# Kernel tuning notes

Measured on AMD Instinct MI355X. Metric: run time of the kernel, lower is better.

Reference implementation:

```python
import jax, jax.numpy as jnp
import numpy as np

B, L, C = 4, 2048, 2048
NH, HD, K = 32, 64, 16  # num_heads, head_dim, inner chunk size
LR = 1.0
EPS = 1e-6


def ln_fwd(x, w, b):
    # F.layer_norm over last dim (biased variance), eps=1e-6
    mu = x.mean(-1, keepdims=True)
    var = x.var(-1, keepdims=True)
    xhat = (x - mu) * jax.lax.rsqrt(var + EPS)
    return w * xhat + b


def ln_fused_l2_bwd(x, target, w, b):
    # grad wrt x of 0.5*||LN(x;w,b) - target||^2 fused with LN fwd
    D = x.shape[-1]
    mu = x.mean(-1, keepdims=True)
    var = x.var(-1, keepdims=True)
    std = jnp.sqrt(var + EPS)
    xhat = (x - mu) / std
    y = w * xhat + b
    g = (y - target) * w  # dL/d(xhat)
    return (D * g - g.sum(-1, keepdims=True) - xhat * (g * xhat).sum(-1, keepdims=True)) / (D * std)


def _inner_scan(XC, XB, XA, coeff, W1, b1, lnw, lnb):
    # per (batch, head): XC/XB/XA [n_chunk,K,HD], coeff [n_chunk,K,1], W1 [HD,HD], b1 [1,HD], lnw/lnb [HD]
    mask = jnp.tril(jnp.ones((K, K), XC.dtype))

    def step(carry, inp):
        W1c, b1c = carry
        xc, xb, xa, co = inp
        Z1 = xb @ W1c + b1c                       # [K,HD]
        grad = ln_fused_l2_bwd(Z1, xa - xb, lnw, lnb)
        Attn1 = mask * (xc @ xb.T)                # [K,K] causal
        b1_bar = b1c - (co * mask) @ grad         # [K,HD]
        Z1_bar = xc @ W1c - (co * Attn1) @ grad + b1_bar
        W1n = W1c - (co[-1] * xb).T @ grad        # fast-weight update with last coeff
        b1n = b1_bar[-1:]
        out = xc + ln_fwd(Z1_bar, lnw, lnb)       # post-LN residual
        return (W1n, b1n), out

    _, ys = jax.lax.scan(step, (W1, b1), (XC, XB, XA, coeff))
    return ys.reshape(-1, HD)  # [L,HD]


def setup_inputs() -> dict:
    key = jax.random.key(0)
    ks = jax.random.split(key, 9)
    s = 0.02
    return {
        'hidden_states': jax.random.normal(ks[0], (B, L, C), jnp.float32),
        'Wq': jax.random.normal(ks[1], (C, NH * HD), jnp.float32) * s,
        'Wk': jax.random.normal(ks[2], (C, NH * HD), jnp.float32) * s,
        'Wv': jax.random.normal(ks[3], (C, NH * HD), jnp.float32) * s,
        'Wo': jax.random.normal(ks[4], (NH * HD, C), jnp.float32) * s,
        'ilr_w': jax.random.normal(ks[5], (C, NH), jnp.float32) * s,
        'ilr_b': jnp.zeros((NH,), jnp.float32),
        'ln_weight': jnp.ones((NH, HD), jnp.float32),
        'ln_bias': jnp.zeros((NH, HD), jnp.float32),
        'W1': jax.random.normal(ks[6], (NH, HD, HD), jnp.float32) * s,
        'b1': jnp.zeros((NH, 1, HD), jnp.float32),
    }


def reference(hidden_states, Wq, Wk, Wv, Wo, ilr_w, ilr_b, ln_weight, ln_bias, W1, b1):
    n_chunk = L // K

    def split(x):  # [B,L,NH*HD] -> [B,NH,n_chunk,K,HD]
        return x.reshape(B, n_chunk, K, NH, HD).transpose(0, 3, 1, 2, 4)

    XC = split(hidden_states @ Wq)
    XB = split(hidden_states @ Wk)
    XA = split(hidden_states @ Wv)

    # sigmoid-gated per-token learning rates
    ilr = jax.nn.sigmoid(hidden_states @ ilr_w + ilr_b)          # [B,L,NH]
    ilr = ilr.reshape(B, n_chunk, K, NH).transpose(0, 3, 1, 2)[..., None]  # [B,NH,n_chunk,K,1]
    token_idx = 1.0 / jnp.arange(1, K + 1, dtype=jnp.float32)
    coeff = (LR * token_idx).reshape(1, 1, 1, K, 1) * ilr / HD

    per_head = jax.vmap(_inner_scan, in_axes=(0, 0, 0, 0, 0, 0, 0, 0))
    per_batch = jax.vmap(per_head, in_axes=(0, 0, 0, 0, None, None, None, None))
    XCW = per_batch(XC, XB, XA, coeff, W1, b1, ln_weight, ln_bias)  # [B,NH,L,HD]
    XCW = XCW.transpose(0, 2, 1, 3).reshape(B, L, NH * HD)
    return XCW @ Wo
```

## Files before the change

kernel.cpp:

```cpp
#include <hip/hip_runtime.h>
#include <hip/hip_bf16.h>

typedef __attribute__((ext_vector_type(8))) short bf16x8;
typedef __attribute__((ext_vector_type(4))) float f32x4;
typedef __attribute__((ext_vector_type(8))) unsigned short u16x8;
typedef __attribute__((ext_vector_type(4))) unsigned short u16x4;
typedef unsigned short u16;

#define AS1(p) ((__attribute__((address_space(1))) void*)(p))
#define AS3(p) ((__attribute__((address_space(3))) void*)(p))
#define GLL16(g, l) __builtin_amdgcn_global_load_lds(AS1(g), AS3(l), 16, 0, 0)

__device__ __forceinline__ u16 f2bf(float x) {
  return __builtin_bit_cast(u16, __float2bfloat16(x));
}
__device__ __forceinline__ float bf2f(u16 u) {
  return __builtin_bit_cast(float, ((unsigned)u) << 16);
}
__device__ __forceinline__ unsigned pk2(float a, float b) {
  return (unsigned)f2bf(a) | ((unsigned)f2bf(b) << 16);
}
__device__ __forceinline__ f32x4 mfma16(bf16x8 a, bf16x8 b, f32x4 c) {
  return __builtin_amdgcn_mfma_f32_16x16x32_bf16(a, b, c, 0, 0, 0);
}
#define DPPADD(x, ctrl)                                                            \
  ((x) + __builtin_bit_cast(float, __builtin_amdgcn_update_dpp(                    \
             0, __builtin_bit_cast(int, (x)), (ctrl), 0xf, 0xf, true)))
__device__ __forceinline__ float rsum16(float x) {
  x = DPPADD(x, 0x128);
  x = DPPADD(x, 0x124);
  x = DPPADD(x, 0x122);
  x = DPPADD(x, 0x121);
  return x;
}
__device__ __forceinline__ void dsfence() { __builtin_amdgcn_sched_barrier(0x7F); }
template <typename T>
__device__ __forceinline__ void lds_st(u16* p, T v) {
  __builtin_memcpy((void*)p, &v, sizeof(T));
}
template <typename T>
__device__ __forceinline__ T lds_ld(const u16* p) {
  T v;
  __builtin_memcpy(&v, (const void*)p, sizeof(T));
  return v;
}

__global__ __launch_bounds__(256) void conv_bf16(const float* __restrict__ in,
                                                 u16* __restrict__ out) {
  size_t g = (size_t)blockIdx.x * 256 + threadIdx.x;
  const float4* p = reinterpret_cast<const float4*>(in) + g * 2;
  float4 a = p[0], b = p[1];
  u16x8 r;
  r[0] = f2bf(a.x); r[1] = f2bf(a.y); r[2] = f2bf(a.z); r[3] = f2bf(a.w);
  r[4] = f2bf(b.x); r[5] = f2bf(b.y); r[6] = f2bf(b.z); r[7] = f2bf(b.w);
  *reinterpret_cast<u16x8*>(out + g * 8) = r;
}

__global__ __launch_bounds__(256) void wt_conv(const float* __restrict__ W,
                                               u16* __restrict__ Wt, int Kd, int N) {
  __shared__ float t[64][65];
  const int n0 = blockIdx.x * 64, k0 = blockIdx.y * 64;
  const int tx = threadIdx.x & 63, ty = threadIdx.x >> 6;
#pragma unroll
  for (int rr = 0; rr < 16; ++rr) {
    int r = rr * 4 + ty;
    t[r][tx] = W[(size_t)(k0 + r) * N + n0 + tx];
  }
  __syncthreads();
#pragma unroll
  for (int rr = 0; rr < 16; ++rr) {
    int r = rr * 4 + ty;
    Wt[(size_t)(n0 + r) * Kd + k0 + tx] = f2bf(t[tx][r]);
  }
}

__global__ __launch_bounds__(256) void ilr_strip(const float* __restrict__ ilr_w,
                                                 u16* __restrict__ WcatT) {
  int g = blockIdx.x * 256 + threadIdx.x;
  int p = g >> 11, k = g & 2047;
  float v = (p < 32) ? ilr_w[k * 32 + p] : 0.f;
  WcatT[(size_t)(6144 + p) * 2048 + k] = f2bf(v);
}

__device__ __forceinline__ void stage_pair(const u16* __restrict__ A, const u16* __restrict__ Bt,
                                           u16* As, u16* Bs, int Kd, int mT, int nT, int kt,
                                           int tid) {
#pragma unroll
  for (int r = 0; r < 2; ++r) {
    int e = r * 2048 + tid * 8;
    int row = e >> 5, kk = e & 31;
    GLL16(A + (size_t)(mT + row) * Kd + kt + kk, As + e);
    GLL16(Bt + (size_t)(nT + row) * Kd + kt + kk, Bs + e);
  }
}

template <int MODE>
__global__ __launch_bounds__(256) void gemm_bt(const u16* __restrict__ A,
                                               const u16* __restrict__ Bt, int M, int N, int Kd,
                                               u16* __restrict__ O0, u16* __restrict__ O1,
                                               u16* __restrict__ O2,
                                               float* __restrict__ coeffOut,
                                               const float* __restrict__ ilrb,
                                               float* __restrict__ Cout) {
  __shared__ __align__(16) u16 As[2][4096];
  __shared__ __align__(16) u16 Bs[2][4096];
  const int tid = threadIdx.x;
  const int lane = tid & 63;
  const int wid = tid >> 6;
  const int wr = wid >> 1, wc = wid & 1;
  const int l15 = lane & 15, l4 = lane >> 4;
  const int mT = blockIdx.y << 7, nT = blockIdx.x << 7;

  f32x4 acc[4][4];
#pragma unroll
  for (int m = 0; m < 4; ++m)
#pragma unroll
    for (int n = 0; n < 4; ++n) acc[m][n] = (f32x4){0.f, 0.f, 0.f, 0.f};

  stage_pair(A, Bt, &As[0][0], &Bs[0][0], Kd, mT, nT, 0, tid);
  const int nIter = Kd >> 5;
  const int aoff = (wr * 64 + l15) * 32 + l4 * 8;
  const int boff = (wc * 64 + l15) * 32 + l4 * 8;
#pragma unroll 1
  for (int it = 0; it < nIter; ++it) {
    const int cur = it & 1;
    __syncthreads();
    if (it + 1 < nIter)
      stage_pair(A, Bt, &As[cur ^ 1][0], &Bs[cur ^ 1][0], Kd, mT, nT, (it + 1) << 5, tid);
    bf16x8 av[4], bv[4];
#pragma unroll
    for (int x = 0; x < 4; ++x) {
      av[x] = *reinterpret_cast<const bf16x8*>(&As[cur][aoff + x * 512]);
      bv[x] = *reinterpret_cast<const bf16x8*>(&Bs[cur][boff + x * 512]);
    }
#pragma unroll
    for (int m = 0; m < 4; ++m)
#pragma unroll
      for (int n = 0; n < 4; ++n) acc[m][n] = mfma16(av[m], bv[n], acc[m][n]);
  }
#pragma unroll
  for (int m = 0; m < 4; ++m) {
#pragma unroll
    for (int n = 0; n < 4; ++n) {
      const int col = nT + wc * 64 + n * 16 + l15;
#pragma unroll
      for (int e = 0; e < 4; ++e) {
        const int row = mT + wr * 64 + m * 16 + l4 * 4 + e;
        float v = acc[m][n][e];
        if constexpr (MODE == 1) {
          Cout[(size_t)row * N + col] = v;
        } else {
          const int bb = row >> 11, lt = row & 2047;
          if (col < 6144) {
            const int mat = col >> 11;
            u16* base = (mat == 0) ? O0 : ((mat == 1) ? O1 : O2);
            const int hh = (col >> 6) & 31, dd = col & 63;
            base[(((size_t)(bb * 32 + hh)) * 2048 + lt) * 64 + dd] = f2bf(v);
          } else {
            const int h3 = col - 6144;
            if (h3 < 32) {
              const float x = v + ilrb[h3];
              const float sig = 1.f / (1.f + expf(-x));
              const int tok = lt & 15;
              coeffOut[((size_t)(bb * 32 + h3)) * 2048 + lt] =
                  sig * (1.f / (64.f * (float)(tok + 1)));
            }
          }
        }
      }
    }
  }
  (void)M;
}

__global__ __launch_bounds__(64) void ttt_scan(
    const u16* __restrict__ XC, const u16* __restrict__ XB, const u16* __restrict__ XA,
    const float* __restrict__ coeff, const float* __restrict__ lnw_g,
    const float* __restrict__ lnb_g, const float* __restrict__ W1g,
    const float* __restrict__ b1g, u16* __restrict__ XCW) {
  const int bh = blockIdx.x;
  const int b = bh >> 5, h = bh & 31;
  const int lane = threadIdx.x & 63;
  const int l15 = lane & 15, l4 = lane >> 4;
  const bool klo = (l4 < 2);

  const u16* xbb = XB + (size_t)bh * 131072;
  const u16* xcb = XC + (size_t)bh * 131072;
  const u16* xab = XA + (size_t)bh * 131072;
  const float* cob = coeff + (size_t)bh * 2048;

  float lnw4[4], lnb4[4], b1m[4];
#pragma unroll
  for (int cb = 0; cb < 4; ++cb) {
    lnw4[cb] = lnw_g[h * 64 + cb * 16 + l15];
    lnb4[cb] = lnb_g[h * 64 + cb * 16 + l15];
    b1m[cb] = b1g[h * 64 + cb * 16 + l15];
  }
  f32x4 mW[4][4];
#pragma unroll
  for (int kb = 0; kb < 4; ++kb)
#pragma unroll
    for (int cb = 0; cb < 4; ++cb)
#pragma unroll
      for (int e = 0; e < 4; ++e)
        mW[kb][cb][e] = W1g[(size_t)h * 4096 + (kb * 16 + l4 * 4 + e) * 64 + cb * 16 + l15];

  __shared__ __align__(16) u16 w1L[64 * 72];
  __shared__ __align__(16) u16 xbTs[64 * 24];
  __shared__ __align__(16) u16 gTs[64 * 24];
  __shared__ __align__(16) u16 ptw[256];

  uint4 nfb0, nfb1, nfc0, nfc1;
  float nco[4], nco15;
  u16 nxa[4][4], nxbC[4][4], nxcC[4][4], nxv[16];
  const int fo = l15 * 128 + l4 * 16;
#define PREFETCH(cc)                                                                 \
  do {                                                                               \
    const char* pb = (const char*)(xbb + (cc) * 1024);                               \
    const char* pc = (const char*)(xcb + (cc) * 1024);                               \
    nfb0 = *(const uint4*)(pb + fo); nfb1 = *(const uint4*)(pb + fo + 64);           \
    nfc0 = *(const uint4*)(pc + fo); nfc1 = *(const uint4*)(pc + fo + 64);           \
    const u16* xap_ = xab + (cc) * 1024;                                             \
    const u16* xbp_ = xbb + (cc) * 1024;                                             \
    const u16* xcp_ = xcb + (cc) * 1024;                                             \
    _Pragma("unroll") for (int cb = 0; cb < 4; ++cb)                                 \
        _Pragma("unroll") for (int e = 0; e < 4; ++e) {                              \
      const int idx = (l4 * 4 + e) * 64 + cb * 16 + l15;                             \
      nxa[cb][e] = xap_[idx];                                                        \
      nxbC[cb][e] = xbp_[idx];                                                       \
      nxcC[cb][e] = xcp_[idx];                                                       \
    }                                                                                \
    _Pragma("unroll") for (int r = 0; r < 16; ++r) nxv[r] = xbp_[r * 64 + lane];     \
    _Pragma("unroll") for (int e = 0; e < 4; ++e) nco[e] = cob[(cc) * 16 + l4 * 4 + e]; \
    nco15 = cob[(cc) * 16 + 15];                                                     \
  } while (0)

  PREFETCH(0);

#pragma unroll 1
  for (int c = 0; c < 128; ++c) {
    const bf16x8 xbr0 = __builtin_bit_cast(bf16x8, nfb0);
    const bf16x8 xbr1 = __builtin_bit_cast(bf16x8, nfb1);
    const bf16x8 xcr0 = __builtin_bit_cast(bf16x8, nfc0);
    const bf16x8 xcr1 = __builtin_bit_cast(bf16x8, nfc1);
    float co_own[4];
#pragma unroll
    for (int e = 0; e < 4; ++e) co_own[e] = nco[e];
    const float co15 = nco15;
    float tgt[4][4], xcC[4][4];
#pragma unroll
    for (int cb = 0; cb < 4; ++cb)
#pragma unroll
      for (int e = 0; e < 4; ++e) {
        tgt[cb][e] = bf2f(nxa[cb][e]) - bf2f(nxbC[cb][e]);
        xcC[cb][e] = bf2f(nxcC[cb][e]);
      }
    u16 xv[16];
#pragma unroll
    for (int r = 0; r < 16; ++r) xv[r] = nxv[r];

    {
      const int cc = (c < 127) ? (c + 1) : 127;
      PREFETCH(cc);
    }

    f32x4 p = {0.f, 0.f, 0.f, 0.f};
    p = mfma16(xcr0, xbr0, p);
    p = mfma16(xcr1, xbr1, p);
#pragma unroll
    for (int e = 0; e < 4; ++e) {
      const int i = l4 * 4 + e;
      const float v = (l15 <= i) ? p[e] * (-co_own[e]) : 0.f;
      lds_st<u16>(&ptw[i * 16 + l15], f2bf(v));
    }

    {
      const float s = -co15;
#pragma unroll
      for (int r2 = 0; r2 < 4; ++r2) {
        u16x4 w;
#pragma unroll
        for (int i = 0; i < 4; ++i) w[i] = f2bf(bf2f(xv[r2 * 4 + i]) * s);
        lds_st<u16x4>(&xbTs[lane * 24 + r2 * 4], w);
      }
    }

#pragma unroll
    for (int kb = 0; kb < 4; ++kb)
#pragma unroll
      for (int cb = 0; cb < 4; ++cb) {
        u16x4 w;
#pragma unroll
        for (int e = 0; e < 4; ++e) w[e] = f2bf(mW[kb][cb][e]);
        lds_st<u16x4>(&w1L[(cb * 16 + l15) * 72 + kb * 16 + l4 * 4], w);
      }
    dsfence();
    bf16x8 w1f[4][2];
#pragma unroll
    for (int cb = 0; cb < 4; ++cb)
#pragma unroll
      for (int s = 0; s < 2; ++s)
        w1f[cb][s] = lds_ld<bf16x8>(&w1L[(cb * 16 + l15) * 72 + s * 32 + l4 * 8]);
    dsfence();

    f32x4 z[4];
#pragma unroll
    for (int cb = 0; cb < 4; ++cb) {
      f32x4 acc = {b1m[cb], b1m[cb], b1m[cb], b1m[cb]};
      acc = mfma16(xbr0, w1f[cb][0], acc);
      z[cb] = mfma16(xbr1, w1f[cb][1], acc);
    }
    f32x4 o2[4];
#pragma unroll
    for (int cb = 0; cb < 4; ++cb) {
      f32x4 acc = {0.f, 0.f, 0.f, 0.f};
      acc = mfma16(xcr0, w1f[cb][0], acc);
      o2[cb] = mfma16(xcr1, w1f[cb][1], acc);
    }

    float xhat[4][4], gr[4][4];
#pragma unroll
    for (int e = 0; e < 4; ++e) {
      float s1 = z[0][e] + z[1][e] + z[2][e] + z[3][e];
      float s2 = z[0][e] * z[0][e] + z[1][e] * z[1][e] + z[2][e] * z[2][e] + z[3][e] * z[3][e];
      s1 = rsum16(s1);
      s2 = rsum16(s2);
      const float mu = s1 * 0.015625f;
      const float var = fmaxf(s2 * 0.015625f - mu * mu, 0.f);
      const float rstd = rsqrtf(var + 1e-6f);
      float gloc[4];
#pragma unroll
      for (int cb = 0; cb < 4; ++cb) {
        xhat[cb][e] = (z[cb][e] - mu) * rstd;
        gloc[cb] = (fmaf(lnw4[cb], xhat[cb][e], lnb4[cb]) - tgt[cb][e]) * lnw4[cb];
      }
      float gs = gloc[0] + gloc[1] + gloc[2] + gloc[3];
      float gx = gloc[0] * xhat[0][e] + gloc[1] * xhat[1][e] + gloc[2] * xhat[2][e] +
                 gloc[3] * xhat[3][e];
      gs = rsum16(gs);
      gx = rsum16(gx);
#pragma unroll
      for (int cb = 0; cb < 4; ++cb)
        gr[cb][e] = (64.f * gloc[cb] - gs - xhat[cb][e] * gx) * (rstd * 0.015625f);
    }

    float gtot[4], lower[4];
#pragma unroll
    for (int cb = 0; cb < 4; ++cb) {
      const float T = gr[cb][0] + gr[cb][1] + gr[cb][2] + gr[cb][3];
      const float t1 = __shfl_xor(T, 16, 64);
      const float t2 = __shfl_xor(T, 32, 64);
      const float t3 = __shfl_xor(t1, 32, 64);
      gtot[cb] = T + t1 + t2 + t3;
      lower[cb] = ((l4 & 1) ? t1 : 0.f) + ((l4 & 2) ? (t2 + t3) : 0.f);
    }

#pragma unroll
    for (int cb = 0; cb < 4; ++cb) {
      uint2 w = {pk2(gr[cb][0], gr[cb][1]), pk2(gr[cb][2], gr[cb][3])};
      lds_st<uint2>(&gTs[(cb * 16 + l15) * 24 + l4 * 4], w);
    }
    dsfence();
    bf16x8 gf[4];
    const bf16x8 zero8 = {};
#pragma unroll
    for (int cb = 0; cb < 4; ++cb) {
      bf16x8 v = lds_ld<bf16x8>(&gTs[(cb * 16 + l15) * 24 + (l4 & 1) * 8]);
      gf[cb] = klo ? v : zero8;
    }
    bf16x8 ptf;
    {
      bf16x8 v = lds_ld<bf16x8>(&ptw[l15 * 16 + (l4 & 1) * 8]);
      ptf = klo ? v : zero8;
    }
    dsfence();

#pragma unroll
    for (int cb = 0; cb < 4; ++cb) o2[cb] = mfma16(ptf, gf[cb], o2[cb]);
    float ov[4][4];
#pragma unroll
    for (int cb = 0; cb < 4; ++cb) {
      float pfx = lower[cb];
#pragma unroll
      for (int e = 0; e < 4; ++e) {
        pfx += gr[cb][e];
        ov[cb][e] = o2[cb][e] + fmaf(-co_own[e], pfx, b1m[cb]);
      }
    }
#pragma unroll
    for (int e = 0; e < 4; ++e) {
      float s1 = ov[0][e] + ov[1][e] + ov[2][e] + ov[3][e];
      float s2 = ov[0][e] * ov[0][e] + ov[1][e] * ov[1][e] + ov[2][e] * ov[2][e] +
                 ov[3][e] * ov[3][e];
      s1 = rsum16(s1);
      s2 = rsum16(s2);
      const float mu = s1 * 0.015625f;
      const float var = fmaxf(s2 * 0.015625f - mu * mu, 0.f);
      const float rstd = rsqrtf(var + 1e-6f);
      const size_t rowg = (size_t)(b * 2048 + c * 16 + l4 * 4 + e) * 2048 + h * 64;
#pragma unroll
      for (int cb = 0; cb < 4; ++cb) {
        const float y = xcC[cb][e] + fmaf(lnw4[cb], (ov[cb][e] - mu) * rstd, lnb4[cb]);
        XCW[rowg + cb * 16 + l15] = f2bf(y);
      }
    }

    bf16x8 xbtf[4];
#pragma unroll
    for (int kb = 0; kb < 4; ++kb) {
      bf16x8 v = lds_ld<bf16x8>(&xbTs[(kb * 16 + l15) * 24 + (l4 & 1) * 8]);
      xbtf[kb] = klo ? v : zero8;
    }
    dsfence();
#pragma unroll
    for (int kb = 0; kb < 4; ++kb)
#pragma unroll
      for (int cb = 0; cb < 4; ++cb) mW[kb][cb] = mfma16(xbtf[kb], gf[cb], mW[kb][cb]);
#pragma unroll
    for (int cb = 0; cb < 4; ++cb) b1m[cb] = fmaf(-co15, gtot[cb], b1m[cb]);
    dsfence();
  }
#undef PREFETCH
}

extern "C" void kernel_launch(void* const* d_in, const int* in_sizes, int n_in, void* d_out,
                              int out_size, void* d_ws, size_t ws_size, hipStream_t stream) {
  const float* hs = (const float*)d_in[0];
  const float* Wq = (const float*)d_in[1];
  const float* Wk = (const float*)d_in[2];
  const float* Wv = (const float*)d_in[3];
  const float* Wo = (const float*)d_in[4];
  const float* ilr_w = (const float*)d_in[5];
  const float* ilr_b = (const float*)d_in[6];
  const float* lnw = (const float*)d_in[7];
  const float* lnb = (const float*)d_in[8];
  const float* W1 = (const float*)d_in[9];
  const float* b1 = (const float*)d_in[10];
  float* out = (float*)d_out;

  if (ws_size < 93847552u) return;
  char* ws = (char*)d_ws;
  u16* hsb = (u16*)(ws + 0);
  u16* WcatT = (u16*)(ws + 33554432);
  u16* XCbf = (u16*)(ws + 59244544);
  float* coeffb = (float*)(ws + 92798976);
  u16* XCW = hsb;
  u16* WoT = (u16*)(ws + 33554432);
  u16* XBbf = (u16*)d_out;
  u16* XAbf = (u16*)((char*)d_out + 33554432);

  conv_bf16<<<8192, 256, 0, stream>>>(hs, hsb);
  wt_conv<<<dim3(32, 32), 256, 0, stream>>>(Wq, WcatT, 2048, 2048);
  wt_conv<<<dim3(32, 32), 256, 0, stream>>>(Wk, WcatT + (size_t)2048 * 2048, 2048, 2048);
  wt_conv<<<dim3(32, 32), 256, 0, stream>>>(Wv, WcatT + (size_t)4096 * 2048, 2048, 2048);
  ilr_strip<<<1024, 256, 0, stream>>>(ilr_w, WcatT);

  gemm_bt<0><<<dim3(49, 64), 256, 0, stream>>>(hsb, WcatT, 8192, 6272, 2048, XCbf, XBbf, XAbf,
                                               coeffb, ilr_b, nullptr);
  wt_conv<<<dim3(32, 32), 256, 0, stream>>>(Wo, WoT, 2048, 2048);
  ttt_scan<<<128, 64, 0, stream>>>(XCbf, XBbf, XAbf, coeffb, lnw, lnb, W1, b1, XCW);
  gemm_bt<1><<<dim3(16, 64), 256, 0, stream>>>(XCW, WoT, 8192, 2048, 2048, nullptr, nullptr,
                                               nullptr, nullptr, nullptr, out);

  (void)in_sizes; (void)n_in; (void)out_size;
}
```

Before: 750.3 us.

## Interleave two independent head sequences per wavefront in TTT scan kernel

The scan kernel now processes two (batch, head) sequences per 64-thread block, with their independent dependency chains interleaved inside one chunk loop, and the grid shrinks from 128 to 64 blocks. The aim is to hide MFMA, LDS and shuffle latency of the serial per-chunk recurrence through instruction-level parallelism across the two streams. The scalar element loads for XA, XB and XC are no longer prefetched one chunk ahead; they are issued in the current iteration. In exchange, only 64 CUs are used instead of 128, register pressure roughly doubles, and the moved loads may expose memory latency.

```diff
diff --git a/kernel.cpp b/kernel.cpp
--- a/kernel.cpp
+++ b/kernel.cpp
@@ -173,254 +173,290 @@
   (void)M;
 }
 
-__global__ __launch_bounds__(64) void ttt_scan(
+__global__ __launch_bounds__(64, 1) void ttt_scan(
     const u16* __restrict__ XC, const u16* __restrict__ XB, const u16* __restrict__ XA,
     const float* __restrict__ coeff, const float* __restrict__ lnw_g,
     const float* __restrict__ lnb_g, const float* __restrict__ W1g,
     const float* __restrict__ b1g, u16* __restrict__ XCW) {
-  const int bh = blockIdx.x;
-  const int b = bh >> 5, h = bh & 31;
+  const int q = blockIdx.x;
+  const int h = q & 31;
   const int lane = threadIdx.x & 63;
   const int l15 = lane & 15, l4 = lane >> 4;
   const bool klo = (l4 < 2);
 
-  const u16* xbb = XB + (size_t)bh * 131072;
-  const u16* xcb = XC + (size_t)bh * 131072;
-  const u16* xab = XA + (size_t)bh * 131072;
-  const float* cob = coeff + (size_t)bh * 2048;
-
-  float lnw4[4], lnb4[4], b1m[4];
+  const u16 *xbb[2], *xcb[2], *xab[2];
+  const float* cob[2];
+  int bseq[2];
+#pragma unroll
+  for (int s = 0; s < 2; ++s) {
+    const int bh = q + s * 64;
+    bseq[s] = bh >> 5;
+    xbb[s] = XB + (size_t)bh * 131072;
+    xcb[s] = XC + (size_t)bh * 131072;
+    xab[s] = XA + (size_t)bh * 131072;
+    cob[s] = coeff + (size_t)bh * 2048;
+  }
+
+  float lnw4[4], lnb4[4];
 #pragma unroll
   for (int cb = 0; cb < 4; ++cb) {
     lnw4[cb] = lnw_g[h * 64 + cb * 16 + l15];
     lnb4[cb] = lnb_g[h * 64 + cb * 16 + l15];
-    b1m[cb] = b1g[h * 64 + cb * 16 + l15];
-  }
-  f32x4 mW[4][4];
-#pragma unroll
-  for (int kb = 0; kb < 4; ++kb)
-#pragma unroll
-    for (int cb = 0; cb < 4; ++cb)
-#pragma unroll
-      for (int e = 0; e < 4; ++e)
-        mW[kb][cb][e] = W1g[(size_t)h * 4096 + (kb * 16 + l4 * 4 + e) * 64 + cb * 16 + l15];
-
-  __shared__ __align__(16) u16 w1L[64 * 72];
-  __shared__ __align__(16) u16 xbTs[64 * 24];
-  __shared__ __align__(16) u16 gTs[64 * 24];
-  __shared__ __align__(16) u16 ptw[256];
-
-  uint4 nfb0, nfb1, nfc0, nfc1;
-  float nco[4], nco15;
-  u16 nxa[4][4], nxbC[4][4], nxcC[4][4], nxv[16];
+  }
+  float b1m[2][4];
+  f32x4 mW[2][4][4];
+#pragma unroll
+  for (int s = 0; s < 2; ++s) {
+#pragma unroll
+    for (int cb = 0; cb < 4; ++cb) b1m[s][cb] = b1g[h * 64 + cb * 16 + l15];
+#pragma unroll
+    for (int kb = 0; kb < 4; ++kb)
+#pragma unroll
+      for (int cb = 0; cb < 4; ++cb)
+#pragma unroll
+        for (int e = 0; e < 4; ++e)
+          mW[s][kb][cb][e] =
+              W1g[(size_t)h * 4096 + (kb * 16 + l4 * 4 + e) * 64 + cb * 16 + l15];
+  }
+
+  __shared__ __align__(16) u16 w1L[2][64 * 72];
+  __shared__ __align__(16) u16 xbTs[2][64 * 24];
+  __shared__ __align__(16) u16 gTs[2][64 * 24];
+  __shared__ __align__(16) u16 ptw[2][256];
+
+  uint4 nfb0[2], nfb1[2], nfc0[2], nfc1[2];
+  float nco[2][4], nco15[2];
   const int fo = l15 * 128 + l4 * 16;
-#define PREFETCH(cc)                                                                 \
-  do {                                                                               \
-    const char* pb = (const char*)(xbb + (cc) * 1024);                               \
-    const char* pc = (const char*)(xcb + (cc) * 1024);                               \
-    nfb0 = *(const uint4*)(pb + fo); nfb1 = *(const uint4*)(pb + fo + 64);           \
-    nfc0 = *(const uint4*)(pc + fo); nfc1 = *(const uint4*)(pc + fo + 64);           \
-    const u16* xap_ = xab + (cc) * 1024;                                             \
-    const u16* xbp_ = xbb + (cc) * 1024;                                             \
-    const u16* xcp_ = xcb + (cc) * 1024;                                             \
-    _Pragma("unroll") for (int cb = 0; cb < 4; ++cb)                                 \
-        _Pragma("unroll") for (int e = 0; e < 4; ++e) {                              \
-      const int idx = (l4 * 4 + e) * 64 + cb * 16 + l15;                             \
-      nxa[cb][e] = xap_[idx];                                                        \
-      nxbC[cb][e] = xbp_[idx];                                                       \
-      nxcC[cb][e] = xcp_[idx];                                                       \
-    }                                                                                \
-    _Pragma("unroll") for (int r = 0; r < 16; ++r) nxv[r] = xbp_[r * 64 + lane];     \
-    _Pragma("unroll") for (int e = 0; e < 4; ++e) nco[e] = cob[(cc) * 16 + l4 * 4 + e]; \
-    nco15 = cob[(cc) * 16 + 15];                                                     \
+#define PFRAG(s, cc)                                                                  \
+  do {                                                                                \
+    const char* pb = (const char*)(xbb[s] + (cc) * 1024);                             \
+    const char* pc = (const char*)(xcb[s] + (cc) * 1024);                             \
+    nfb0[s] = *(const uint4*)(pb + fo); nfb1[s] = *(const uint4*)(pb + fo + 64);      \
+    nfc0[s] = *(const uint4*)(pc + fo); nfc1[s] = *(const uint4*)(pc + fo + 64);      \
+    _Pragma("unroll") for (int e = 0; e < 4; ++e)                                     \
+        nco[s][e] = cob[s][(cc) * 16 + l4 * 4 + e];                                   \
+    nco15[s] = cob[s][(cc) * 16 + 15];                                                \
   } while (0)
 
-  PREFETCH(0);
+#pragma unroll
+  for (int s = 0; s < 2; ++s) PFRAG(s, 0);
 
 #pragma unroll 1
   for (int c = 0; c < 128; ++c) {
-    const bf16x8 xbr0 = __builtin_bit_cast(bf16x8, nfb0);
-    const bf16x8 xbr1 = __builtin_bit_cast(bf16x8, nfb1);
-    const bf16x8 xcr0 = __builtin_bit_cast(bf16x8, nfc0);
-    const bf16x8 xcr1 = __builtin_bit_cast(bf16x8, nfc1);
-    float co_own[4];
-#pragma unroll
-    for (int e = 0; e < 4; ++e) co_own[e] = nco[e];
-    const float co15 = nco15;
-    float tgt[4][4], xcC[4][4];
-#pragma unroll
-    for (int cb = 0; cb < 4; ++cb)
-#pragma unroll
-      for (int e = 0; e < 4; ++e) {
-        tgt[cb][e] = bf2f(nxa[cb][e]) - bf2f(nxbC[cb][e]);
-        xcC[cb][e] = bf2f(nxcC[cb][e]);
-      }
-    u16 xv[16];
-#pragma unroll
-    for (int r = 0; r < 16; ++r) xv[r] = nxv[r];
+    bf16x8 xbr0[2], xbr1[2], xcr0[2], xcr1[2];
+    float co_own[2][4], co15[2];
+#pragma unroll
+    for (int s = 0; s < 2; ++s) {
+      xbr0[s] = __builtin_bit_cast(bf16x8, nfb0[s]);
+      xbr1[s] = __builtin_bit_cast(bf16x8, nfb1[s]);
+      xcr0[s] = __builtin_bit_cast(bf16x8, nfc0[s]);
+      xcr1[s] = __builtin_bit_cast(bf16x8, nfc1[s]);
+#pragma unroll
+      for (int e = 0; e < 4; ++e) co_own[s][e] = nco[s][e];
+      co15[s] = nco15[s];
+    }
+
+    u16 sxa[2][4][4], sxb[2][4][4], sxc[2][4][4], sxv[2][16];
+#pragma unroll
+    for (int s = 0; s < 2; ++s) {
+      const u16* xap_ = xab[s] + c * 1024;
+      const u16* xbp_ = xbb[s] + c * 1024;
+      const u16* xcp_ = xcb[s] + c * 1024;
+#pragma unroll
+      for (int cb = 0; cb < 4; ++cb)
+#pragma unroll
+        for (int e = 0; e < 4; ++e) {
+          const int idx = (l4 * 4 + e) * 64 + cb * 16 + l15;
+          sxa[s][cb][e] = xap_[idx];
+          sxb[s][cb][e] = xbp_[idx];
+          sxc[s][cb][e] = xcp_[idx];
+        }
+#pragma unroll
+      for (int r = 0; r < 16; ++r) sxv[s][r] = xbp_[r * 64 + lane];
+    }
 
     {
       const int cc = (c < 127) ? (c + 1) : 127;
-      PREFETCH(cc);
-    }
-
-    f32x4 p = {0.f, 0.f, 0.f, 0.f};
-    p = mfma16(xcr0, xbr0, p);
-    p = mfma16(xcr1, xbr1, p);
-#pragma unroll
-    for (int e = 0; e < 4; ++e) {
-      const int i = l4 * 4 + e;
-      const float v = (l15 <= i) ? p[e] * (-co_own[e]) : 0.f;
-      lds_st<u16>(&ptw[i * 16 + l15], f2bf(v));
-    }
-
-    {
-      const float s = -co15;
+#pragma unroll
+      for (int s = 0; s < 2; ++s) PFRAG(s, cc);
+    }
+
+#pragma unroll
+    for (int s = 0; s < 2; ++s) {
+      f32x4 p = {0.f, 0.f, 0.f, 0.f};
+      p = mfma16(xcr0[s], xbr0[s], p);
+      p = mfma16(xcr1[s], xbr1[s], p);
+#pragma unroll
+      for (int e = 0; e < 4; ++e) {
+        const int i = l4 * 4 + e;
+        const float v = (l15 <= i) ? p[e] * (-co_own[s][e]) : 0.f;
+        lds_st<u16>(&ptw[s][i * 16 + l15], f2bf(v));
+      }
+    }
+
+#pragma unroll
+    for (int s = 0; s < 2; ++s)
+#pragma unroll
+      for (int kb = 0; kb < 4; ++kb)
+#pragma unroll
+        for (int cb = 0; cb < 4; ++cb) {
+          u16x4 w;
+#pragma unroll
+          for (int e = 0; e < 4; ++e) w[e] = f2bf(mW[s][kb][cb][e]);
+          lds_st<u16x4>(&w1L[s][(cb * 16 + l15) * 72 + kb * 16 + l4 * 4], w);
+        }
+    dsfence();
+    f32x4 z[2][4], o2[2][4];
+#pragma unroll
+    for (int s = 0; s < 2; ++s) {
+      bf16x8 w1f[4][2];
+#pragma unroll
+      for (int cb = 0; cb < 4; ++cb)
+#pragma unroll
+        for (int t = 0; t < 2; ++t)
+          w1f[cb][t] = lds_ld<bf16x8>(&w1L[s][(cb * 16 + l15) * 72 + t * 32 + l4 * 8]);
+#pragma unroll
+      for (int cb = 0; cb < 4; ++cb) {
+        f32x4 a = {b1m[s][cb], b1m[s][cb], b1m[s][cb], b1m[s][cb]};
+        a = mfma16(xbr0[s], w1f[cb][0], a);
+        z[s][cb] = mfma16(xbr1[s], w1f[cb][1], a);
+        f32x4 a2 = {0.f, 0.f, 0.f, 0.f};
+        a2 = mfma16(xcr0[s], w1f[cb][0], a2);
+        o2[s][cb] = mfma16(xcr1[s], w1f[cb][1], a2);
+      }
+    }
+    dsfence();
+
+    float gr[2][4][4];
+#pragma unroll
+    for (int s = 0; s < 2; ++s) {
+#pragma unroll
+      for (int e = 0; e < 4; ++e) {
+        float zz[4];
+#pragma unroll
+        for (int cb = 0; cb < 4; ++cb) zz[cb] = z[s][cb][e];
+        float s1 = zz[0] + zz[1] + zz[2] + zz[3];
+        float s2 = zz[0] * zz[0] + zz[1] * zz[1] + zz[2] * zz[2] + zz[3] * zz[3];
+        s1 = rsum16(s1);
+        s2 = rsum16(s2);
+        const float mu = s1 * 0.015625f;
+        const float var = fmaxf(s2 * 0.015625f - mu * mu, 0.f);
+        const float rstd = rsqrtf(var + 1e-6f);
+        float xh[4], gl[4];
+#pragma unroll
+        for (int cb = 0; cb < 4; ++cb) {
+          xh[cb] = (zz[cb] - mu) * rstd;
+          const float tgt = bf2f(sxa[s][cb][e]) - bf2f(sxb[s][cb][e]);
+          gl[cb] = (fmaf(lnw4[cb], xh[cb], lnb4[cb]) - tgt) * lnw4[cb];
+        }
+        float gs = gl[0] + gl[1] + gl[2] + gl[3];
+        float gx = gl[0] * xh[0] + gl[1] * xh[1] + gl[2] * xh[2] + gl[3] * xh[3];
+        gs = rsum16(gs);
+        gx = rsum16(gx);
+#pragma unroll
+        for (int cb = 0; cb < 4; ++cb)
+          gr[s][cb][e] = (64.f * gl[cb] - gs - xh[cb] * gx) * (rstd * 0.015625f);
+      }
+    }
+
+    float gtot[2][4], lower[2][4];
+#pragma unroll
+    for (int s = 0; s < 2; ++s)
+#pragma unroll
+      for (int cb = 0; cb < 4; ++cb) {
+        const float T = gr[s][cb][0] + gr[s][cb][1] + gr[s][cb][2] + gr[s][cb][3];
+        const float t1 = __shfl_xor(T, 16, 64);
+        const float t2 = __shfl_xor(T, 32, 64);
+        const float t3 = __shfl_xor(t1, 32, 64);
+        gtot[s][cb] = T + t1 + t2 + t3;
+        lower[s][cb] = ((l4 & 1) ? t1 : 0.f) + ((l4 & 2) ? (t2 + t3) : 0.f);
+      }
+
+#pragma unroll
+    for (int s = 0; s < 2; ++s) {
+      const float sc = -co15[s];
 #pragma unroll
       for (int r2 = 0; r2 < 4; ++r2) {
         u16x4 w;
 #pragma unroll
-        for (int i = 0; i < 4; ++i) w[i] = f2bf(bf2f(xv[r2 * 4 + i]) * s);
-        lds_st<u16x4>(&xbTs[lane * 24 + r2 * 4], w);
-      }
-    }
-
-#pragma unroll
-    for (int kb = 0; kb < 4; ++kb)
+        for (int i = 0; i < 4; ++i) w[i] = f2bf(bf2f(sxv[s][r2 * 4 + i]) * sc);
+        lds_st<u16x4>(&xbTs[s][lane * 24 + r2 * 4], w);
+      }
 #pragma unroll
       for (int cb = 0; cb < 4; ++cb) {
-        u16x4 w;
-#pragma unroll
-        for (int e = 0; e < 4; ++e) w[e] = f2bf(mW[kb][cb][e]);
-        lds_st<u16x4>(&w1L[(cb * 16 + l15) * 72 + kb * 16 + l4 * 4], w);
-      }
+        uint2 w = {pk2(gr[s][cb][0], gr[s][cb][1]), pk2(gr[s][cb][2], gr[s][cb][3])};
+        lds_st<uint2>(&gTs[s][(cb * 16 + l15) * 24 + l4 * 4], w);
+      }
+    }
     dsfence();
-    bf16x8 w1f[4][2];
-#pragma unroll
-    for (int cb = 0; cb < 4; ++cb)
-#pragma unroll
-      for (int s = 0; s < 2; ++s)
-        w1f[cb][s] = lds_ld<bf16x8>(&w1L[(cb * 16 + l15) * 72 + s * 32 + l4 * 8]);
+    bf16x8 gf[2][4], ptf[2], xbtf[2][4];
+    const bf16x8 zero8 = {};
+#pragma unroll
+    for (int s = 0; s < 2; ++s) {
+#pragma unroll
+      for (int cb = 0; cb < 4; ++cb) {
+        bf16x8 v = lds_ld<bf16x8>(&gTs[s][(cb * 16 + l15) * 24 + (l4 & 1) * 8]);
+        gf[s][cb] = klo ? v : zero8;
+      }
+      {
+        bf16x8 v = lds_ld<bf16x8>(&ptw[s][l15 * 16 + (l4 & 1) * 8]);
+        ptf[s] = klo ? v : zero8;
+      }
+#pragma unroll
+      for (int kb = 0; kb < 4; ++kb) {
+        bf16x8 v = lds_ld<bf16x8>(&xbTs[s][(kb * 16 + l15) * 24 + (l4 & 1) * 8]);
+        xbtf[s][kb] = klo ? v : zero8;
+      }
+    }
     dsfence();
 
-    f32x4 z[4];
-#pragma unroll
-    for (int cb = 0; cb < 4; ++cb) {
-      f32x4 acc = {b1m[cb], b1m[cb], b1m[cb], b1m[cb]};
-      acc = mfma16(xbr0, w1f[cb][0], acc);
-      z[cb] = mfma16(xbr1, w1f[cb][1], acc);
-    }
-    f32x4 o2[4];
-#pragma unroll
-    for (int cb = 0; cb < 4; ++cb) {
-      f32x4 acc = {0.f, 0.f, 0.f, 0.f};
-      acc = mfma16(xcr0, w1f[cb][0], acc);
-      o2[cb] = mfma16(xcr1, w1f[cb][1], acc);
-    }
-
-    float xhat[4][4], gr[4][4];
-#pragma unroll
-    for (int e = 0; e < 4; ++e) {
-      float s1 = z[0][e] + z[1][e] + z[2][e] + z[3][e];
-      float s2 = z[0][e] * z[0][e] + z[1][e] * z[1][e] + z[2][e] * z[2][e] + z[3][e] * z[3][e];
-      s1 = rsum16(s1);
-      s2 = rsum16(s2);
-      const float mu = s1 * 0.015625f;
-      const float var = fmaxf(s2 * 0.015625f - mu * mu, 0.f);
-      const float rstd = rsqrtf(var + 1e-6f);
-      float gloc[4];
+#pragma unroll
+    for (int s = 0; s < 2; ++s) {
+#pragma unroll
+      for (int cb = 0; cb < 4; ++cb) o2[s][cb] = mfma16(ptf[s], gf[s][cb], o2[s][cb]);
+      float ov[4][4];
 #pragma unroll
       for (int cb = 0; cb < 4; ++cb) {
-        xhat[cb][e] = (z[cb][e] - mu) * rstd;
-        gloc[cb] = (fmaf(lnw4[cb], xhat[cb][e], lnb4[cb]) - tgt[cb][e]) * lnw4[cb];
-      }
-      float gs = gloc[0] + gloc[1] + gloc[2] + gloc[3];
-      float gx = gloc[0] * xhat[0][e] + gloc[1] * xhat[1][e] + gloc[2] * xhat[2][e] +
-                 gloc[3] * xhat[3][e];
-      gs = rsum16(gs);
-      gx = rsum16(gx);
-#pragma unroll
-      for (int cb = 0; cb < 4; ++cb)
-        gr[cb][e] = (64.f * gloc[cb] - gs - xhat[cb][e] * gx) * (rstd * 0.015625f);
-    }
-
-    float gtot[4], lower[4];
-#pragma unroll
-    for (int cb = 0; cb < 4; ++cb) {
-      const float T = gr[cb][0] + gr[cb][1] + gr[cb][2] + gr[cb][3];
-      const float t1 = __shfl_xor(T, 16, 64);
-      const float t2 = __shfl_xor(T, 32, 64);
-      const float t3 = __shfl_xor(t1, 32, 64);
-      gtot[cb] = T + t1 + t2 + t3;
-      lower[cb] = ((l4 & 1) ? t1 : 0.f) + ((l4 & 2) ? (t2 + t3) : 0.f);
-    }
-
-#pragma unroll
-    for (int cb = 0; cb < 4; ++cb) {
-      uint2 w = {pk2(gr[cb][0], gr[cb][1]), pk2(gr[cb][2], gr[cb][3])};
-      lds_st<uint2>(&gTs[(cb * 16 + l15) * 24 + l4 * 4], w);
+        float pfx = lower[s][cb];
+#pragma unroll
+        for (int e = 0; e < 4; ++e) {
+          pfx += gr[s][cb][e];
+          ov[cb][e] = o2[s][cb][e] + fmaf(-co_own[s][e], pfx, b1m[s][cb]);
+        }
+      }
+#pragma unroll
+      for (int e = 0; e < 4; ++e) {
+        float s1 = ov[0][e] + ov[1][e] + ov[2][e] + ov[3][e];
+        float s2 = ov[0][e] * ov[0][e] + ov[1][e] * ov[1][e] + ov[2][e] * ov[2][e] +
+                   ov[3][e] * ov[3][e];
+        s1 = rsum16(s1);
+        s2 = rsum16(s2);
+        const float mu = s1 * 0.015625f;
+        const float var = fmaxf(s2 * 0.015625f - mu * mu, 0.f);
+        const float rstd = rsqrtf(var + 1e-6f);
+        const size_t rowg = (size_t)(bseq[s] * 2048 + c * 16 + l4 * 4 + e) * 2048 + h * 64;
+#pragma unroll
+        for (int cb = 0; cb < 4; ++cb) {
+          const float y =
+              bf2f(sxc[s][cb][e]) + fmaf(lnw4[cb], (ov[cb][e] - mu) * rstd, lnb4[cb]);
+          XCW[rowg + cb * 16 + l15] = f2bf(y);
+        }
+      }
+    }
+
+#pragma unroll
+    for (int s = 0; s < 2; ++s) {
+#pragma unroll
+      for (int kb = 0; kb < 4; ++kb)
+#pragma unroll
+        for (int cb = 0; cb < 4; ++cb)
+          mW[s][kb][cb] = mfma16(xbtf[s][kb], gf[s][cb], mW[s][kb][cb]);
+#pragma unroll
+      for (int cb = 0; cb < 4; ++cb) b1m[s][cb] = fmaf(-co15[s], gtot[s][cb], b1m[s][cb]);
     }
     dsfence();
-    bf16x8 gf[4];
-    const bf16x8 zero8 = {};
-#pragma unroll
-    for (int cb = 0; cb < 4; ++cb) {
-      bf16x8 v = lds_ld<bf16x8>(&gTs[(cb * 16 + l15) * 24 + (l4 & 1) * 8]);
-      gf[cb] = klo ? v : zero8;
-    }
-    bf16x8 ptf;
-    {
-      bf16x8 v = lds_ld<bf16x8>(&ptw[l15 * 16 + (l4 & 1) * 8]);
-      ptf = klo ? v : zero8;
-    }
-    dsfence();
-
-#pragma unroll
-    for (int cb = 0; cb < 4; ++cb) o2[cb] = mfma16(ptf, gf[cb], o2[cb]);
-    float ov[4][4];
-#pragma unroll
-    for (int cb = 0; cb < 4; ++cb) {
-      float pfx = lower[cb];
-#pragma unroll
-      for (int e = 0; e < 4; ++e) {
-        pfx += gr[cb][e];
-        ov[cb][e] = o2[cb][e] + fmaf(-co_own[e], pfx, b1m[cb]);
-      }
-    }
-#pragma unroll
-    for (int e = 0; e < 4; ++e) {
-      float s1 = ov[0][e] + ov[1][e] + ov[2][e] + ov[3][e];
-      float s2 = ov[0][e] * ov[0][e] + ov[1][e] * ov[1][e] + ov[2][e] * ov[2][e] +
-                 ov[3][e] * ov[3][e];
-      s1 = rsum16(s1);
-      s2 = rsum16(s2);
-      const float mu = s1 * 0.015625f;
-      const float var = fmaxf(s2 * 0.015625f - mu * mu, 0.f);
-      const float rstd = rsqrtf(var + 1e-6f);
-      const size_t rowg = (size_t)(b * 2048 + c * 16 + l4 * 4 + e) * 2048 + h * 64;
-#pragma unroll
-      for (int cb = 0; cb < 4; ++cb) {
-        const float y = xcC[cb][e] + fmaf(lnw4[cb], (ov[cb][e] - mu) * rstd, lnb4[cb]);
-        XCW[rowg + cb * 16 + l15] = f2bf(y);
-      }
-    }
-
-    bf16x8 xbtf[4];
-#pragma unroll
-    for (int kb = 0; kb < 4; ++kb) {
-      bf16x8 v = lds_ld<bf16x8>(&xbTs[(kb * 16 + l15) * 24 + (l4 & 1) * 8]);
-      xbtf[kb] = klo ? v : zero8;
-    }
-    dsfence();
-#pragma unroll
-    for (int kb = 0; kb < 4; ++kb)
-#pragma unroll
-      for (int cb = 0; cb < 4; ++cb) mW[kb][cb] = mfma16(xbtf[kb], gf[cb], mW[kb][cb]);
-#pragma unroll
-    for (int cb = 0; cb < 4; ++cb) b1m[cb] = fmaf(-co15, gtot[cb], b1m[cb]);
-    dsfence();
-  }
-#undef PREFETCH
+  }
+#undef PFRAG
 }
 
 extern "C" void kernel_launch(void* const* d_in, const int* in_sizes, int n_in, void* d_out,
@@ -458,7 +494,7 @@
   gemm_bt<0><<<dim3(49, 64), 256, 0, stream>>>(hsb, WcatT, 8192, 6272, 2048, XCbf, XBbf, XAbf,
                                                coeffb, ilr_b, nullptr);
   wt_conv<<<dim3(32, 32), 256, 0, stream>>>(Wo, WoT, 2048, 2048);
-  ttt_scan<<<128, 64, 0, stream>>>(XCbf, XBbf, XAbf, coeffb, lnw, lnb, W1, b1, XCW);
+  ttt_scan<<<64, 64, 0, stream>>>(XCbf, XBbf, XAbf, coeffb, lnw, lnb, W1, b1, XCW);
   gemm_bt<1><<<dim3(16, 64), 256, 0, stream>>>(XCW, WoT, 8192, 2048, 2048, nullptr, nullptr,
                                                nullptr, nullptr, nullptr, out);
 
```

Result: slower. 1.054 ms (+40.5%).

## Use 16x16x16 bf16 MFMA with register-resident operands to eliminate LDS staging in TTT scan

Applied to the files above, without the earlier changes.

Rewrites the per-chunk inner scan to use the K=16 MFMA variant, whose operand layout matches the accumulator layout. This lets W1, the gradient, the causal attention tile and the scaled XB feed the next MFMAs straight from registers instead of going through LDS transposes and sched barriers. Removing the LDS round-trips and fences shortens the serial per-chunk critical path. In exchange it issues more MFMA instructions (the K=16 shape instead of K=32), and the elementwise XA/XB/XC loads are no longer prefetched one chunk ahead.

```diff
diff --git a/kernel.cpp b/kernel.cpp
--- a/kernel.cpp
+++ b/kernel.cpp
@@ -2,9 +2,9 @@
 #include <hip/hip_bf16.h>
 
 typedef __attribute__((ext_vector_type(8))) short bf16x8;
+typedef __attribute__((ext_vector_type(4))) short bf16x4;
 typedef __attribute__((ext_vector_type(4))) float f32x4;
 typedef __attribute__((ext_vector_type(8))) unsigned short u16x8;
-typedef __attribute__((ext_vector_type(4))) unsigned short u16x4;
 typedef unsigned short u16;
 
 #define AS1(p) ((__attribute__((address_space(1))) void*)(p))
@@ -17,11 +17,24 @@
 __device__ __forceinline__ float bf2f(u16 u) {
   return __builtin_bit_cast(float, ((unsigned)u) << 16);
 }
-__device__ __forceinline__ unsigned pk2(float a, float b) {
-  return (unsigned)f2bf(a) | ((unsigned)f2bf(b) << 16);
-}
 __device__ __forceinline__ f32x4 mfma16(bf16x8 a, bf16x8 b, f32x4 c) {
   return __builtin_amdgcn_mfma_f32_16x16x32_bf16(a, b, c, 0, 0, 0);
+}
+__device__ __forceinline__ f32x4 mfma16k(bf16x4 a, bf16x4 b, f32x4 c) {
+#if defined(__HIP_DEVICE_COMPILE__)
+#if __has_builtin(__builtin_amdgcn_mfma_f32_16x16x16bf16_1k)
+  return __builtin_amdgcn_mfma_f32_16x16x16bf16_1k(a, b, c, 0, 0, 0);
+#else
+  f32x4 d;
+  asm volatile("v_mfma_f32_16x16x16_bf16 %0, %1, %2, %3"
+               : "=v"(d)
+               : "v"(a), "v"(b), "v"(c));
+  return d;
+#endif
+#else
+  (void)a; (void)b;
+  return c;
+#endif
 }
 #define DPPADD(x, ctrl)                                                            \
   ((x) + __builtin_bit_cast(float, __builtin_amdgcn_update_dpp(                    \
@@ -32,17 +45,6 @@
   x = DPPADD(x, 0x122);
   x = DPPADD(x, 0x121);
   return x;
-}
-__device__ __forceinline__ void dsfence() { __builtin_amdgcn_sched_barrier(0x7F); }
-template <typename T>
-__device__ __forceinline__ void lds_st(u16* p, T v) {
-  __builtin_memcpy((void*)p, &v, sizeof(T));
-}
-template <typename T>
-__device__ __forceinline__ T lds_ld(const u16* p) {
-  T v;
-  __builtin_memcpy(&v, (const void*)p, sizeof(T));
-  return v;
 }
 
 __global__ __launch_bounds__(256) void conv_bf16(const float* __restrict__ in,
@@ -182,7 +184,6 @@
   const int b = bh >> 5, h = bh & 31;
   const int lane = threadIdx.x & 63;
   const int l15 = lane & 15, l4 = lane >> 4;
-  const bool klo = (l4 < 2);
 
   const u16* xbb = XB + (size_t)bh * 131072;
   const u16* xcb = XC + (size_t)bh * 131072;
@@ -205,143 +206,112 @@
       for (int e = 0; e < 4; ++e)
         mW[kb][cb][e] = W1g[(size_t)h * 4096 + (kb * 16 + l4 * 4 + e) * 64 + cb * 16 + l15];
 
-  __shared__ __align__(16) u16 w1L[64 * 72];
-  __shared__ __align__(16) u16 xbTs[64 * 24];
-  __shared__ __align__(16) u16 gTs[64 * 24];
-  __shared__ __align__(16) u16 ptw[256];
-
-  uint4 nfb0, nfb1, nfc0, nfc1;
-  float nco[4], nco15;
-  u16 nxa[4][4], nxbC[4][4], nxcC[4][4], nxv[16];
-  const int fo = l15 * 128 + l4 * 16;
-#define PREFETCH(cc)                                                                 \
+  uint2 nxbA[4], nxcA[4];
+  float nco[4], nco15, ncoL;
+  const int foA = l15 * 128 + l4 * 8;
+#define PF(cc)                                                                       \
   do {                                                                               \
     const char* pb = (const char*)(xbb + (cc) * 1024);                               \
     const char* pc = (const char*)(xcb + (cc) * 1024);                               \
-    nfb0 = *(const uint4*)(pb + fo); nfb1 = *(const uint4*)(pb + fo + 64);           \
-    nfc0 = *(const uint4*)(pc + fo); nfc1 = *(const uint4*)(pc + fo + 64);           \
-    const u16* xap_ = xab + (cc) * 1024;                                             \
-    const u16* xbp_ = xbb + (cc) * 1024;                                             \
-    const u16* xcp_ = xcb + (cc) * 1024;                                             \
-    _Pragma("unroll") for (int cb = 0; cb < 4; ++cb)                                 \
-        _Pragma("unroll") for (int e = 0; e < 4; ++e) {                              \
-      const int idx = (l4 * 4 + e) * 64 + cb * 16 + l15;                             \
-      nxa[cb][e] = xap_[idx];                                                        \
-      nxbC[cb][e] = xbp_[idx];                                                       \
-      nxcC[cb][e] = xcp_[idx];                                                       \
+    _Pragma("unroll") for (int kb = 0; kb < 4; ++kb) {                               \
+      nxbA[kb] = *(const uint2*)(pb + foA + kb * 32);                                \
+      nxcA[kb] = *(const uint2*)(pc + foA + kb * 32);                                \
     }                                                                                \
-    _Pragma("unroll") for (int r = 0; r < 16; ++r) nxv[r] = xbp_[r * 64 + lane];     \
     _Pragma("unroll") for (int e = 0; e < 4; ++e) nco[e] = cob[(cc) * 16 + l4 * 4 + e]; \
     nco15 = cob[(cc) * 16 + 15];                                                     \
+    ncoL = cob[(cc) * 16 + l15];                                                     \
   } while (0)
 
-  PREFETCH(0);
+  PF(0);
 
 #pragma unroll 1
   for (int c = 0; c < 128; ++c) {
-    const bf16x8 xbr0 = __builtin_bit_cast(bf16x8, nfb0);
-    const bf16x8 xbr1 = __builtin_bit_cast(bf16x8, nfb1);
-    const bf16x8 xcr0 = __builtin_bit_cast(bf16x8, nfc0);
-    const bf16x8 xcr1 = __builtin_bit_cast(bf16x8, nfc1);
+    bf16x4 xbA[4], xcA[4];
+#pragma unroll
+    for (int kb = 0; kb < 4; ++kb) {
+      xbA[kb] = __builtin_bit_cast(bf16x4, nxbA[kb]);
+      xcA[kb] = __builtin_bit_cast(bf16x4, nxcA[kb]);
+    }
     float co_own[4];
 #pragma unroll
     for (int e = 0; e < 4; ++e) co_own[e] = nco[e];
-    const float co15 = nco15;
-    float tgt[4][4], xcC[4][4];
-#pragma unroll
-    for (int cb = 0; cb < 4; ++cb)
-#pragma unroll
-      for (int e = 0; e < 4; ++e) {
-        tgt[cb][e] = bf2f(nxa[cb][e]) - bf2f(nxbC[cb][e]);
-        xcC[cb][e] = bf2f(nxcC[cb][e]);
-      }
-    u16 xv[16];
-#pragma unroll
-    for (int r = 0; r < 16; ++r) xv[r] = nxv[r];
-
+    const float co15 = nco15, coL = ncoL;
+
+    u16 sxa[4][4], sxb[4][4], sxc[4][4];
     {
-      const int cc = (c < 127) ? (c + 1) : 127;
-      PREFETCH(cc);
-    }
-
-    f32x4 p = {0.f, 0.f, 0.f, 0.f};
-    p = mfma16(xcr0, xbr0, p);
-    p = mfma16(xcr1, xbr1, p);
+      const u16* xap_ = xab + c * 1024;
+      const u16* xbp_ = xbb + c * 1024;
+      const u16* xcp_ = xcb + c * 1024;
+#pragma unroll
+      for (int cb = 0; cb < 4; ++cb)
+#pragma unroll
+        for (int e = 0; e < 4; ++e) {
+          const int idx = (l4 * 4 + e) * 64 + cb * 16 + l15;
+          sxa[cb][e] = xap_[idx];
+          sxb[cb][e] = xbp_[idx];
+          sxc[cb][e] = xcp_[idx];
+        }
+    }
+    PF((c < 127) ? (c + 1) : 127);
+
+    f32x4 pT = {0.f, 0.f, 0.f, 0.f};
+#pragma unroll
+    for (int kb = 0; kb < 4; ++kb) pT = mfma16k(xbA[kb], xcA[kb], pT);
+    bf16x4 pTf;
 #pragma unroll
     for (int e = 0; e < 4; ++e) {
-      const int i = l4 * 4 + e;
-      const float v = (l15 <= i) ? p[e] * (-co_own[e]) : 0.f;
-      lds_st<u16>(&ptw[i * 16 + l15], f2bf(v));
-    }
-
-    {
-      const float s = -co15;
-#pragma unroll
-      for (int r2 = 0; r2 < 4; ++r2) {
-        u16x4 w;
-#pragma unroll
-        for (int i = 0; i < 4; ++i) w[i] = f2bf(bf2f(xv[r2 * 4 + i]) * s);
-        lds_st<u16x4>(&xbTs[lane * 24 + r2 * 4], w);
-      }
-    }
-
+      const int r = l4 * 4 + e;
+      pTf[e] = (short)f2bf((r <= l15) ? pT[e] * (-coL) : 0.f);
+    }
+
+    bf16x4 w1b[4][4];
 #pragma unroll
     for (int kb = 0; kb < 4; ++kb)
 #pragma unroll
-      for (int cb = 0; cb < 4; ++cb) {
-        u16x4 w;
-#pragma unroll
-        for (int e = 0; e < 4; ++e) w[e] = f2bf(mW[kb][cb][e]);
-        lds_st<u16x4>(&w1L[(cb * 16 + l15) * 72 + kb * 16 + l4 * 4], w);
-      }
-    dsfence();
-    bf16x8 w1f[4][2];
-#pragma unroll
-    for (int cb = 0; cb < 4; ++cb)
-#pragma unroll
-      for (int s = 0; s < 2; ++s)
-        w1f[cb][s] = lds_ld<bf16x8>(&w1L[(cb * 16 + l15) * 72 + s * 32 + l4 * 8]);
-    dsfence();
-
-    f32x4 z[4];
+      for (int cb = 0; cb < 4; ++cb)
+#pragma unroll
+        for (int e = 0; e < 4; ++e) w1b[kb][cb][e] = (short)f2bf(mW[kb][cb][e]);
+
+    f32x4 z[4], o2[4];
 #pragma unroll
     for (int cb = 0; cb < 4; ++cb) {
-      f32x4 acc = {b1m[cb], b1m[cb], b1m[cb], b1m[cb]};
-      acc = mfma16(xbr0, w1f[cb][0], acc);
-      z[cb] = mfma16(xbr1, w1f[cb][1], acc);
-    }
-    f32x4 o2[4];
-#pragma unroll
-    for (int cb = 0; cb < 4; ++cb) {
-      f32x4 acc = {0.f, 0.f, 0.f, 0.f};
-      acc = mfma16(xcr0, w1f[cb][0], acc);
-      o2[cb] = mfma16(xcr1, w1f[cb][1], acc);
-    }
-
-    float xhat[4][4], gr[4][4];
+      f32x4 a = {b1m[cb], b1m[cb], b1m[cb], b1m[cb]};
+#pragma unroll
+      for (int kb = 0; kb < 4; ++kb) a = mfma16k(xbA[kb], w1b[kb][cb], a);
+      z[cb] = a;
+      f32x4 a2 = {0.f, 0.f, 0.f, 0.f};
+#pragma unroll
+      for (int kb = 0; kb < 4; ++kb) a2 = mfma16k(xcA[kb], w1b[kb][cb], a2);
+      o2[cb] = a2;
+    }
+
+    float gr[4][4];
 #pragma unroll
     for (int e = 0; e < 4; ++e) {
-      float s1 = z[0][e] + z[1][e] + z[2][e] + z[3][e];
-      float s2 = z[0][e] * z[0][e] + z[1][e] * z[1][e] + z[2][e] * z[2][e] + z[3][e] * z[3][e];
+      float zz[4];
+#pragma unroll
+      for (int cb = 0; cb < 4; ++cb) zz[cb] = z[cb][e];
+      float s1 = zz[0] + zz[1] + zz[2] + zz[3];
+      float s2 = zz[0] * zz[0] + zz[1] * zz[1] + zz[2] * zz[2] + zz[3] * zz[3];
       s1 = rsum16(s1);
       s2 = rsum16(s2);
       const float mu = s1 * 0.015625f;
       const float var = fmaxf(s2 * 0.015625f - mu * mu, 0.f);
       const float rstd = rsqrtf(var + 1e-6f);
-      float gloc[4];
+      float xh[4], gl[4];
 #pragma unroll
       for (int cb = 0; cb < 4; ++cb) {
-        xhat[cb][e] = (z[cb][e] - mu) * rstd;
-        gloc[cb] = (fmaf(lnw4[cb], xhat[cb][e], lnb4[cb]) - tgt[cb][e]) * lnw4[cb];
+        xh[cb] = (zz[cb] - mu) * rstd;
+        const float tgt = bf2f(sxa[cb][e]) - bf2f(sxb[cb][e]);
+        gl[cb] = (fmaf(lnw4[cb], xh[cb], lnb4[cb]) - tgt) * lnw4[cb];
       }
-      float gs = gloc[0] + gloc[1] + gloc[2] + gloc[3];
-      float gx = gloc[0] * xhat[0][e] + gloc[1] * xhat[1][e] + gloc[2] * xhat[2][e] +
-                 gloc[3] * xhat[3][e];
+      float gs = gl[0] + gl[1] + gl[2] + gl[3];
+      float gx = gl[0] * xh[0] + gl[1] * xh[1] + gl[2] * xh[2] + gl[3] * xh[3];
       gs = rsum16(gs);
       gx = rsum16(gx);
 #pragma unroll
       for (int cb = 0; cb < 4; ++cb)
-        gr[cb][e] = (64.f * gloc[cb] - gs - xhat[cb][e] * gx) * (rstd * 0.015625f);
+        gr[cb][e] = (64.f * gl[cb] - gs - xh[cb] * gx) * (rstd * 0.015625f);
     }
 
     float gtot[4], lower[4];
@@ -355,28 +325,26 @@
       lower[cb] = ((l4 & 1) ? t1 : 0.f) + ((l4 & 2) ? (t2 + t3) : 0.f);
     }
 
-#pragma unroll
-    for (int cb = 0; cb < 4; ++cb) {
-      uint2 w = {pk2(gr[cb][0], gr[cb][1]), pk2(gr[cb][2], gr[cb][3])};
-      lds_st<uint2>(&gTs[(cb * 16 + l15) * 24 + l4 * 4], w);
-    }
-    dsfence();
-    bf16x8 gf[4];
-    const bf16x8 zero8 = {};
-#pragma unroll
-    for (int cb = 0; cb < 4; ++cb) {
-      bf16x8 v = lds_ld<bf16x8>(&gTs[(cb * 16 + l15) * 24 + (l4 & 1) * 8]);
-      gf[cb] = klo ? v : zero8;
-    }
-    bf16x8 ptf;
-    {
-      bf16x8 v = lds_ld<bf16x8>(&ptw[l15 * 16 + (l4 & 1) * 8]);
-      ptf = klo ? v : zero8;
-    }
-    dsfence();
-
-#pragma unroll
-    for (int cb = 0; cb < 4; ++cb) o2[cb] = mfma16(ptf, gf[cb], o2[cb]);
+    bf16x4 grB[4];
+#pragma unroll
+    for (int cb = 0; cb < 4; ++cb)
+#pragma unroll
+      for (int e = 0; e < 4; ++e) grB[cb][e] = (short)f2bf(gr[cb][e]);
+
+#pragma unroll
+    for (int cb = 0; cb < 4; ++cb) o2[cb] = mfma16k(pTf, grB[cb], o2[cb]);
+
+    bf16x4 xbU[4];
+#pragma unroll
+    for (int kb = 0; kb < 4; ++kb)
+#pragma unroll
+      for (int e = 0; e < 4; ++e)
+        xbU[kb][e] = (short)f2bf(bf2f(sxb[kb][e]) * (-co15));
+#pragma unroll
+    for (int kb = 0; kb < 4; ++kb)
+#pragma unroll
+      for (int cb = 0; cb < 4; ++cb) mW[kb][cb] = mfma16k(xbU[kb], grB[cb], mW[kb][cb]);
+
     float ov[4][4];
 #pragma unroll
     for (int cb = 0; cb < 4; ++cb) {
@@ -400,27 +368,15 @@
       const size_t rowg = (size_t)(b * 2048 + c * 16 + l4 * 4 + e) * 2048 + h * 64;
 #pragma unroll
       for (int cb = 0; cb < 4; ++cb) {
-        const float y = xcC[cb][e] + fmaf(lnw4[cb], (ov[cb][e] - mu) * rstd, lnb4[cb]);
+        const float y = bf2f(sxc[cb][e]) + fmaf(lnw4[cb], (ov[cb][e] - mu) * rstd, lnb4[cb]);
         XCW[rowg + cb * 16 + l15] = f2bf(y);
       }
     }
 
-    bf16x8 xbtf[4];
-#pragma unroll
-    for (int kb = 0; kb < 4; ++kb) {
-      bf16x8 v = lds_ld<bf16x8>(&xbTs[(kb * 16 + l15) * 24 + (l4 & 1) * 8]);
-      xbtf[kb] = klo ? v : zero8;
-    }
-    dsfence();
-#pragma unroll
-    for (int kb = 0; kb < 4; ++kb)
-#pragma unroll
-      for (int cb = 0; cb < 4; ++cb) mW[kb][cb] = mfma16(xbtf[kb], gf[cb], mW[kb][cb]);
 #pragma unroll
     for (int cb = 0; cb < 4; ++cb) b1m[cb] = fmaf(-co15, gtot[cb], b1m[cb]);
-    dsfence();
-  }
-#undef PREFETCH
+  }
+#undef PF
 }
 
 extern "C" void kernel_launch(void* const* d_in, const int* in_sizes, int n_in, void* d_out,
```

Result: faster. 715.9 us (-4.6%).
